# Kernel tuning notes

Measured on AMD Instinct MI355X. Metric: run time of the kernel, lower is better.

## Reference

```python
import jax, jax.numpy as jnp
import numpy as np

N_NODES = 50000


def gcn_conv(x, src, dst, W, b, n_nodes):
    """PyG GCNConv: linear -> sym-normalized aggregation with self-loops -> bias."""
    h = x @ W  # [N, out]
    # add self loops
    loop = jnp.arange(n_nodes, dtype=src.dtype)
    src_f = jnp.concatenate([src, loop])
    dst_f = jnp.concatenate([dst, loop])
    # degree at target nodes (edge weight = 1)
    deg = jax.ops.segment_sum(jnp.ones_like(dst_f, dtype=h.dtype), dst_f, num_segments=n_nodes)
    dinv = jnp.where(deg > 0, jax.lax.rsqrt(deg), 0.0)
    norm = dinv[src_f] * dinv[dst_f]  # [E+N]
    msg = h[src_f] * norm[:, None]    # gather + scale
    out = jax.ops.segment_sum(msg, dst_f, num_segments=n_nodes)
    return out + b


def setup_inputs() -> dict:
    key = jax.random.key(0)
    k1, k2, k3, k4 = jax.random.split(key, 4)
    N, F, H, C, E = N_NODES, 512, 256, 16, 800000
    x = jax.random.normal(k1, (N, F), dtype=jnp.float32)
    edge_index = jax.random.randint(k2, (2, E), 0, N, dtype=jnp.int64)
    W1 = jax.random.normal(k3, (F, H), dtype=jnp.float32) * (1.0 / np.sqrt(F))
    b1 = jnp.zeros((H,), dtype=jnp.float32)
    W2 = jax.random.normal(k4, (H, C), dtype=jnp.float32) * (1.0 / np.sqrt(H))
    b2 = jnp.zeros((C,), dtype=jnp.float32)
    return {"x": x, "edge_index": edge_index, "W1": W1, "b1": b1, "W2": W2, "b2": b2}


def reference(x, edge_index, W1, b1, W2, b2):
    src, dst = edge_index[0], edge_index[1]
    h = gcn_conv(x, src, dst, W1, b1, N_NODES)
    h = jax.nn.relu(h)
    # F.dropout with training=False (eval mode) is identity
    out = gcn_conv(h, src, dst, W2, b2, N_NODES)
    return out
```

## Files before the change

### kernel.cpp

```cpp
#include <hip/hip_runtime.h>
#include <stdint.h>

#define N_NODES 50000
#define N_PAD   50048
#define F_IN 512
#define H_DIM 256
#define C_DIM 16

typedef __attribute__((ext_vector_type(8))) short short8;
typedef __attribute__((ext_vector_type(4))) float f32x4;
typedef __attribute__((ext_vector_type(4))) unsigned short us4;
typedef __attribute__((ext_vector_type(8))) unsigned short us8;

__device__ inline float bf2f(unsigned short u) {
    return __uint_as_float(((uint32_t)u) << 16);
}
__device__ inline unsigned short f2bf(float f) {
    uint32_t u = __float_as_uint(f);
    u += 0x7FFFu + ((u >> 16) & 1u);
    return (unsigned short)(u >> 16);
}
__device__ inline unsigned short hx(float f) {
    return (unsigned short)(__float_as_uint(f) >> 16);
}
__device__ inline int eidx(const void* p, long long i, int is64) {
    return is64 ? (int)((const long long*)p)[i] : ((const int*)p)[i];
}

__device__ inline int row_beg(const int* ro, const int* bs, int n) {
    return ro[n] + bs[n >> 9];
}
__device__ inline int row_end(const int* ro, const int* bs, int n, int E) {
    return (n + 1 < N_NODES) ? ro[n + 1] + bs[(n + 1) >> 9] : E;
}

#define GLOAD16(gp, lp)                                                       \
    __builtin_amdgcn_global_load_lds(                                         \
        (const __attribute__((address_space(1))) void*)(gp),                  \
        (__attribute__((address_space(3))) void*)(lp), 16, 0, 0)


__global__ void prep_k(const void* ei, int* flag,
                       const float* w1, unsigned short* w1t,
                       const float* w2, unsigned short* w2t,
                       int* cnt, int* cur) {
    int i = blockIdx.x * 256 + threadIdx.x;
    if (i == 0) {
        const uint32_t* w = (const uint32_t*)ei;
        int is64 = 1;
        for (int j = 1; j < 128; j += 2)
            if (w[j] != 0u) { is64 = 0; break; }
        *flag = is64;
    }
    if (i < N_NODES) { cnt[i] = 0; cur[i] = 0; }
    if (i < F_IN * H_DIM) {
        int k = i / H_DIM, n = i % H_DIM;
        w1t[n * F_IN + k] = f2bf(w1[i]);
    }
    if (i < H_DIM * C_DIM) {
        int k = i / C_DIM, n = i % C_DIM;
        w2t[n * H_DIM + k] = f2bf(w2[i]);
    }
}


__global__ void hist_k(const void* ei, const int* flag, int* cnt, long long E) {
    long long e = (long long)blockIdx.x * 256 + threadIdx.x;
    if (e >= E) return;
    int d = eidx(ei, E + e, *flag);
    atomicAdd(&cnt[d], 1);
}

__global__ __launch_bounds__(512) void scan1_k(const int* cnt, int* rowoff, int* bsum,
                                               float* dinv, int n) {
    __shared__ int s[512];
    int t = threadIdx.x;
    int i = blockIdx.x * 512 + t;
    int v = (i < n) ? cnt[i] : 0;
    s[t] = v;
    __syncthreads();
    for (int off = 1; off < 512; off <<= 1) {
        int add = (t >= off) ? s[t - off] : 0;
        __syncthreads();
        s[t] += add;
        __syncthreads();
    }
    if (i < n) {
        rowoff[i] = s[t] - v;
        dinv[i] = rsqrtf((float)(v + 1));
    }
    if (t == 511) bsum[blockIdx.x] = s[511];
}

__global__ void scan2_k(int* bsum, int nb) {
    __shared__ int s[128];
    int t = threadIdx.x;
    int v = (t < nb) ? bsum[t] : 0;
    s[t] = v;
    __syncthreads();
    for (int off = 1; off < 128; off <<= 1) {
        int add = (t >= off) ? s[t - off] : 0;
        __syncthreads();
        s[t] += add;
        __syncthreads();
    }
    if (t < nb) bsum[t] = s[t] - v;
}

__global__ void scatter_k(const void* ei, const int* flag, const float* dinv,
                          const int* rowoff, const int* bsum, int* cur,
                          long long E, int2* colnorm) {
    long long e = (long long)blockIdx.x * 256 + threadIdx.x;
    if (e >= E) return;
    int is64 = *flag;
    int s = eidx(ei, e, is64);
    int d = eidx(ei, E + e, is64);
    int pos = row_beg(rowoff, bsum, d) + atomicAdd(&cur[d], 1);
    float nrm = dinv[s] * dinv[d];
    int2 cn;
    cn.x = s;
    cn.y = __float_as_int(nrm);
    colnorm[pos] = cn;
}


__global__ __launch_bounds__(512, 4) void gemm1_k(const float* __restrict__ x,
                                                  const unsigned short* __restrict__ w1t,
                                                  unsigned short* __restrict__ h1) {
    __shared__ __align__(16) float          Asf[2][128 * 32];
    __shared__ __align__(16) unsigned short Bs[2][256 * 32];

    const int t = threadIdx.x;
    const int wv = t >> 6, lane = t & 63;
    const int lg = lane >> 4, lr = lane & 15;
    const int wm = wv >> 2, wn = wv & 3;

    const int arow0 = t >> 3;
    const int achk = (t & 7) ^ (arow0 & 7);
    size_t g0 = (size_t)blockIdx.x * 128 + arow0;
    size_t g1 = g0 + 64;
    if (g0 > N_NODES - 1) g0 = N_NODES - 1;
    if (g1 > N_NODES - 1) g1 = N_NODES - 1;
    const float* asrc0 = x + g0 * F_IN + achk * 4;
    const float* asrc1 = x + g1 * F_IN + achk * 4;
    const unsigned short* bsrc0 = w1t + (size_t)(t >> 2) * F_IN + (t & 3) * 8;
    const unsigned short* bsrc1 = bsrc0 + 128 * F_IN;

#define STAGE(bf, ks)                                                         \
    do { const int _o = (ks) * 32;                                            \
        GLOAD16(asrc0 + _o, &Asf[bf][t * 4]);                                 \
        GLOAD16(asrc1 + _o, &Asf[bf][t * 4 + 2048]);                          \
        GLOAD16(bsrc0 + _o, &Bs[bf][t * 8]);                                  \
        GLOAD16(bsrc1 + _o, &Bs[bf][(t + 512) * 8]);                          \
    } while (0)

    f32x4 acc[4][4] = {};

    STAGE(0, 0);

    for (int ks = 0; ks < 16; ++ks) {
        const int bf = ks & 1;
        if (ks < 15) {
            STAGE(bf ^ 1, ks + 1);
            asm volatile("s_waitcnt vmcnt(4)" ::: "memory");
        } else {
            asm volatile("s_waitcnt vmcnt(0)" ::: "memory");
        }
        __builtin_amdgcn_sched_barrier(0);
        __builtin_amdgcn_s_barrier();

        short8 afr[4], bfr[4];
#pragma unroll
        for (int mi = 0; mi < 4; ++mi) {
            const int r = wm * 64 + mi * 16 + lr;
            const int s = r & 7;
            const float* base = &Asf[bf][r * 32];
            f32x4 lo = *(const f32x4*)(base + (((lg * 2) ^ s) * 4));
            f32x4 hi = *(const f32x4*)(base + (((lg * 2 + 1) ^ s) * 4));
            short8 a;
            a[0] = (short)hx(lo[0]); a[1] = (short)hx(lo[1]);
            a[2] = (short)hx(lo[2]); a[3] = (short)hx(lo[3]);
            a[4] = (short)hx(hi[0]); a[5] = (short)hx(hi[1]);
            a[6] = (short)hx(hi[2]); a[7] = (short)hx(hi[3]);
            afr[mi] = a;
        }
#pragma unroll
        for (int ni = 0; ni < 4; ++ni)
            bfr[ni] = *(const short8*)&Bs[bf][(wn * 64 + ni * 16 + lr) * 32 + lg * 8];
#pragma unroll
        for (int mi = 0; mi < 4; ++mi)
#pragma unroll
            for (int ni = 0; ni < 4; ++ni)
                acc[mi][ni] = __builtin_amdgcn_mfma_f32_16x16x32_bf16(
                    afr[mi], bfr[ni], acc[mi][ni], 0, 0, 0);

        asm volatile("s_waitcnt lgkmcnt(0)" ::: "memory");
        __builtin_amdgcn_sched_barrier(0);
        __builtin_amdgcn_s_barrier();
    }
#undef STAGE

    const size_t rbase = (size_t)blockIdx.x * 128 + wm * 64 + lg * 4;
#pragma unroll
    for (int mi = 0; mi < 4; ++mi)
#pragma unroll
        for (int ni = 0; ni < 4; ++ni)
#pragma unroll
            for (int j = 0; j < 4; ++j)
                h1[(rbase + mi * 16 + j) * H_DIM + wn * 64 + ni * 16 + lr] =
                    f2bf(acc[mi][ni][j]);
}


__global__ __launch_bounds__(256) void agg1_k(const unsigned short* __restrict__ h1,
                                              const int* __restrict__ rowoff,
                                              const int* __restrict__ bsum,
                                              const int2* __restrict__ colnorm,
                                              const float* __restrict__ dinv,
                                              const float* __restrict__ b1,
                                              unsigned short* __restrict__ h1a,
                                              int E) {
    int wv = threadIdx.x >> 6, lane = threadIdx.x & 63;
    int node = blockIdx.x * 4 + wv;
    if (node >= N_NODES) return;
    int half = lane >> 5;
    int fl = (lane & 31) * 8;
    int beg = row_beg(rowoff, bsum, node);
    int end = row_end(rowoff, bsum, node, E);
    float a[8] = {0.f, 0.f, 0.f, 0.f, 0.f, 0.f, 0.f, 0.f};
    const unsigned short* base = h1 + fl;

    int e = beg + half;
    while (e + 6 < end) {
        int2 c[4];
        us8 v[4];
#pragma unroll
        for (int q = 0; q < 4; ++q) c[q] = colnorm[e + q * 2];
#pragma unroll
        for (int q = 0; q < 4; ++q)
            v[q] = *(const us8*)(base + (long long)c[q].x * H_DIM);
#pragma unroll
        for (int q = 0; q < 4; ++q) {
            float n = __int_as_float(c[q].y);
#pragma unroll
            for (int j = 0; j < 8; ++j) a[j] += n * bf2f(v[q][j]);
        }
        e += 8;
    }
    while (e < end) {
        int2 c0 = colnorm[e];
        us8 v0 = *(const us8*)(base + (long long)c0.x * H_DIM);
        float n0 = __int_as_float(c0.y);
#pragma unroll
        for (int j = 0; j < 8; ++j) a[j] += n0 * bf2f(v0[j]);
        e += 2;
    }
#pragma unroll
    for (int j = 0; j < 8; ++j)
        a[j] += __shfl_xor(a[j], 32);

    if (half == 0) {
        float dn = dinv[node];
        float sn = dn * dn;
        us8 vs = *(const us8*)(base + (long long)node * H_DIM);
        float4 b0 = *(const float4*)(b1 + fl);
        float4 b4 = *(const float4*)(b1 + fl + 4);
        float bb[8] = {b0.x, b0.y, b0.z, b0.w, b4.x, b4.y, b4.z, b4.w};
        us8 o;
#pragma unroll
        for (int j = 0; j < 8; ++j) {
            float r = fmaxf(a[j] + sn * bf2f(vs[j]) + bb[j], 0.f);
            o[j] = f2bf(r);
        }
        *(us8*)(h1a + (long long)node * H_DIM + fl) = o;
    }
}


__global__ __launch_bounds__(256) void gemm2_k(const unsigned short* __restrict__ h1a,
                                               const unsigned short* __restrict__ w2t,
                                               float* __restrict__ h2) {
    int t = threadIdx.x;
    int wv = t >> 6, lane = t & 63, lg = lane >> 4, lr = lane & 15;
    int rbase = blockIdx.x * 64 + wv * 16;
    int rr = rbase + lr;
    int rc = rr < N_NODES ? rr : N_NODES - 1;
    f32x4 acc = {0.f, 0.f, 0.f, 0.f};
#pragma unroll
    for (int ks = 0; ks < 8; ++ks) {
        short8 a = *(const short8*)(h1a + (long long)rc * H_DIM + ks * 32 + lg * 8);
        short8 b = *(const short8*)(w2t + lr * H_DIM + ks * 32 + lg * 8);
        acc = __builtin_amdgcn_mfma_f32_16x16x32_bf16(a, b, acc, 0, 0, 0);
    }
#pragma unroll
    for (int j = 0; j < 4; ++j) {
        int row = rbase + lg * 4 + j;
        if (row < N_NODES) h2[(long long)row * C_DIM + lr] = acc[j];
    }
}


__global__ __launch_bounds__(256) void agg2_k(const float* __restrict__ h2,
                                              const int* __restrict__ rowoff,
                                              const int* __restrict__ bsum,
                                              const int2* __restrict__ colnorm,
                                              const float* __restrict__ dinv,
                                              const float* __restrict__ b2,
                                              float* __restrict__ out, int E) {
    int g = threadIdx.x >> 4, c = threadIdx.x & 15;
    int node = blockIdx.x * 16 + g;
    if (node >= N_NODES) return;
    int beg = row_beg(rowoff, bsum, node);
    int end = row_end(rowoff, bsum, node, E);
    float acc = 0.f;
    int e = beg;
    for (; e + 3 < end; e += 4) {
        int2 cn0 = colnorm[e];
        int2 cn1 = colnorm[e + 1];
        int2 cn2 = colnorm[e + 2];
        int2 cn3 = colnorm[e + 3];
        float v0 = h2[(long long)cn0.x * C_DIM + c];
        float v1 = h2[(long long)cn1.x * C_DIM + c];
        float v2 = h2[(long long)cn2.x * C_DIM + c];
        float v3 = h2[(long long)cn3.x * C_DIM + c];
        acc += __int_as_float(cn0.y) * v0 + __int_as_float(cn1.y) * v1
             + __int_as_float(cn2.y) * v2 + __int_as_float(cn3.y) * v3;
    }
    for (; e < end; ++e) {
        int2 cn = colnorm[e];
        acc += __int_as_float(cn.y) * h2[(long long)cn.x * C_DIM + c];
    }
    float dn = dinv[node];
    acc += dn * dn * h2[(long long)node * C_DIM + c];
    out[(long long)node * C_DIM + c] = acc + b2[c];
}


extern "C" void kernel_launch(void* const* d_in, const int* in_sizes, int n_in,
                              void* d_out, int out_size, void* d_ws, size_t ws_size,
                              hipStream_t stream) {
    const float* x  = (const float*)d_in[0];
    const void*  ei = d_in[1];
    const float* W1 = (const float*)d_in[2];
    const float* b1 = (const float*)d_in[3];
    const float* W2 = (const float*)d_in[4];
    const float* b2 = (const float*)d_in[5];
    float* out = (float*)d_out;
    long long E = (long long)in_sizes[1] / 2;

    char* w = (char*)d_ws;
    auto alloc = [&](size_t bytes) -> char* {
        char* p = w;
        w += (bytes + 255) & ~(size_t)255;
        return p;
    };
    int*   flag    = (int*)   alloc(4);
    int*   cnt     = (int*)   alloc((size_t)N_NODES * 4);
    int*   cur     = (int*)   alloc((size_t)N_NODES * 4);
    float* dinv    = (float*) alloc((size_t)N_NODES * 4);
    int*   rowoff  = (int*)   alloc((size_t)N_NODES * 4);
    int*   bsum    = (int*)   alloc(512 * 4);
    int2*  colnorm = (int2*)  alloc((size_t)E * 8);
    unsigned short* w1t = (unsigned short*)alloc((size_t)H_DIM * F_IN * 2);
    unsigned short* w2t = (unsigned short*)alloc((size_t)C_DIM * H_DIM * 2);
    unsigned short* h1  = (unsigned short*)alloc((size_t)N_PAD * H_DIM * 2);
    unsigned short* h1a = (unsigned short*)alloc((size_t)N_NODES * H_DIM * 2);
    float* h2 = (float*)alloc((size_t)N_NODES * C_DIM * 4);

    prep_k<<<(F_IN * H_DIM + 255) / 256, 256, 0, stream>>>(ei, flag, W1, w1t, W2, w2t,
                                                           cnt, cur);

    int egrid = (int)((E + 255) / 256);
    hist_k<<<egrid, 256, 0, stream>>>(ei, flag, cnt, E);
    int sgrid = (N_NODES + 511) / 512;
    scan1_k<<<sgrid, 512, 0, stream>>>(cnt, rowoff, bsum, dinv, N_NODES);
    scan2_k<<<1, 128, 0, stream>>>(bsum, sgrid);
    scatter_k<<<egrid, 256, 0, stream>>>(ei, flag, dinv, rowoff, bsum, cur, E, colnorm);

    gemm1_k<<<N_PAD / 128, 512, 0, stream>>>(x, w1t, h1);
    agg1_k<<<(N_NODES + 3) / 4, 256, 0, stream>>>(h1, rowoff, bsum, colnorm, dinv,
                                                  b1, h1a, (int)E);
    gemm2_k<<<(N_NODES + 63) / 64, 256, 0, stream>>>(h1a, w2t, h2);
    agg2_k<<<(N_NODES + 15) / 16, 256, 0, stream>>>(h2, rowoff, bsum, colnorm, dinv,
                                                    b2, out, (int)E);
}
```

Measured before the change: 202.2 us.

## Fold block-sum scan into scan1 and co-launch edge scatter with GEMM1

Removes the separate scan2 kernel by having the last-finishing scan1 block serially compute the exclusive prefix of block sums, using a done counter and thread fences. It also merges the CSR scatter into the GEMM1 launch as extra blocks, so the latency-bound atomic scatter can overlap with the compute-bound GEMM. This cuts two kernel launches and their gaps. The cost is a serial single-thread scan over about 98 entries and heavy LDS allocation on scatter blocks, which could limit their occupancy.

```diff
diff --git a/kernel.cpp b/kernel.cpp
--- a/kernel.cpp
+++ b/kernel.cpp
@@ -6,6 +6,7 @@
 #define F_IN 512
 #define H_DIM 256
 #define C_DIM 16
+#define G1_BLOCKS (N_PAD / 128)
 
 typedef __attribute__((ext_vector_type(8))) short short8;
 typedef __attribute__((ext_vector_type(4))) float f32x4;
@@ -43,7 +44,7 @@
 __global__ void prep_k(const void* ei, int* flag,
                        const float* w1, unsigned short* w1t,
                        const float* w2, unsigned short* w2t,
-                       int* cnt, int* cur) {
+                       int* cnt, int* cur, int* done) {
     int i = blockIdx.x * 256 + threadIdx.x;
     if (i == 0) {
         const uint32_t* w = (const uint32_t*)ei;
@@ -51,6 +52,7 @@
         for (int j = 1; j < 128; j += 2)
             if (w[j] != 0u) { is64 = 0; break; }
         *flag = is64;
+        *done = 0;
     }
     if (i < N_NODES) { cnt[i] = 0; cur[i] = 0; }
     if (i < F_IN * H_DIM) {
@@ -72,8 +74,9 @@
 }
 
 __global__ __launch_bounds__(512) void scan1_k(const int* cnt, int* rowoff, int* bsum,
-                                               float* dinv, int n) {
+                                               float* dinv, int* done, int n, int nblk) {
     __shared__ int s[512];
+    __shared__ int amLast;
     int t = threadIdx.x;
     int i = blockIdx.x * 512 + t;
     int v = (i < n) ? cnt[i] : 0;
@@ -90,45 +93,47 @@
         dinv[i] = rsqrtf((float)(v + 1));
     }
     if (t == 511) bsum[blockIdx.x] = s[511];
-}
-
-__global__ void scan2_k(int* bsum, int nb) {
-    __shared__ int s[128];
-    int t = threadIdx.x;
-    int v = (t < nb) ? bsum[t] : 0;
-    s[t] = v;
+    __threadfence();
+    if (t == 0) amLast = (atomicAdd(done, 1) == nblk - 1);
     __syncthreads();
-    for (int off = 1; off < 128; off <<= 1) {
-        int add = (t >= off) ? s[t - off] : 0;
-        __syncthreads();
-        s[t] += add;
-        __syncthreads();
-    }
-    if (t < nb) bsum[t] = s[t] - v;
-}
-
-__global__ void scatter_k(const void* ei, const int* flag, const float* dinv,
-                          const int* rowoff, const int* bsum, int* cur,
-                          long long E, int2* colnorm) {
-    long long e = (long long)blockIdx.x * 256 + threadIdx.x;
-    if (e >= E) return;
-    int is64 = *flag;
-    int s = eidx(ei, e, is64);
-    int d = eidx(ei, E + e, is64);
-    int pos = row_beg(rowoff, bsum, d) + atomicAdd(&cur[d], 1);
-    float nrm = dinv[s] * dinv[d];
-    int2 cn;
-    cn.x = s;
-    cn.y = __float_as_int(nrm);
-    colnorm[pos] = cn;
-}
-
-
-__global__ __launch_bounds__(512, 4) void gemm1_k(const float* __restrict__ x,
-                                                  const unsigned short* __restrict__ w1t,
-                                                  unsigned short* __restrict__ h1) {
+    if (amLast && t == 0) {
+        __threadfence();
+        volatile int* vb = bsum;
+        int run = 0;
+        for (int b = 0; b < nblk; ++b) {
+            int x = vb[b];
+            vb[b] = run;
+            run += x;
+        }
+    }
+}
+
+
+__global__ __launch_bounds__(512, 4) void gemm1scat_k(
+        const float* __restrict__ x, const unsigned short* __restrict__ w1t,
+        unsigned short* __restrict__ h1,
+        const void* __restrict__ ei, const int* __restrict__ flag,
+        const float* __restrict__ dinv, const int* __restrict__ rowoff,
+        const int* __restrict__ bsum, int* __restrict__ cur,
+        long long E, int2* __restrict__ colnorm) {
     __shared__ __align__(16) float          Asf[2][128 * 32];
     __shared__ __align__(16) unsigned short Bs[2][256 * 32];
+
+    if (blockIdx.x >= G1_BLOCKS) {
+        long long e = (long long)(blockIdx.x - G1_BLOCKS) * 512 + threadIdx.x;
+        if (e < E) {
+            int is64 = *flag;
+            int s = eidx(ei, e, is64);
+            int d = eidx(ei, E + e, is64);
+            int pos = row_beg(rowoff, bsum, d) + atomicAdd(&cur[d], 1);
+            float nrm = dinv[s] * dinv[d];
+            int2 cn;
+            cn.x = s;
+            cn.y = __float_as_int(nrm);
+            colnorm[pos] = cn;
+        }
+        return;
+    }
 
     const int t = threadIdx.x;
     const int wv = t >> 6, lane = t & 63;
@@ -354,7 +359,8 @@
         w += (bytes + 255) & ~(size_t)255;
         return p;
     };
-    int*   flag    = (int*)   alloc(4);
+    int*   flag    = (int*)   alloc(8);
+    int*   done    = flag + 1;
     int*   cnt     = (int*)   alloc((size_t)N_NODES * 4);
     int*   cur     = (int*)   alloc((size_t)N_NODES * 4);
     float* dinv    = (float*) alloc((size_t)N_NODES * 4);
@@ -368,16 +374,17 @@
     float* h2 = (float*)alloc((size_t)N_NODES * C_DIM * 4);
 
     prep_k<<<(F_IN * H_DIM + 255) / 256, 256, 0, stream>>>(ei, flag, W1, w1t, W2, w2t,
-                                                           cnt, cur);
+                                                           cnt, cur, done);
 
     int egrid = (int)((E + 255) / 256);
     hist_k<<<egrid, 256, 0, stream>>>(ei, flag, cnt, E);
     int sgrid = (N_NODES + 511) / 512;
-    scan1_k<<<sgrid, 512, 0, stream>>>(cnt, rowoff, bsum, dinv, N_NODES);
-    scan2_k<<<1, 128, 0, stream>>>(bsum, sgrid);
-    scatter_k<<<egrid, 256, 0, stream>>>(ei, flag, dinv, rowoff, bsum, cur, E, colnorm);
-
-    gemm1_k<<<N_PAD / 128, 512, 0, stream>>>(x, w1t, h1);
+    scan1_k<<<sgrid, 512, 0, stream>>>(cnt, rowoff, bsum, dinv, done, N_NODES, sgrid);
+
+    int scgrid = (int)((E + 511) / 512);
+    gemm1scat_k<<<G1_BLOCKS + scgrid, 512, 0, stream>>>(
+        x, w1t, h1, ei, flag, dinv, rowoff, bsum, cur, E, colnorm);
+
     agg1_k<<<(N_NODES + 3) / 4, 256, 0, stream>>>(h1, rowoff, bsum, colnorm, dinv,
                                                   b1, h1a, (int)E);
     gemm2_k<<<(N_NODES + 63) / 64, 256, 0, stream>>>(h1a, w2t, h2);
```

Result: slower. 250.1 us (+23.7%).

## Split hidden features into 32-column slabs so gather aggregation stays cache-resident

Applied to the files above, without the earlier changes.

Stores the first-layer hidden matrix as eight feature slabs of 32 columns each, rather than row-major 256-wide rows. The first aggregation kernel launches eight times as many blocks, and each block gathers only from one slab (about 3.2 MB), so the random neighbour gathers can hit in cache. The second GEMM and the GEMM1 epilogue are adapted to the new layout, and edge-list loads and output stores use nontemporal hints. In exchange, the CSR column list is re-read once per slab (eight times in total), and each gather is now a small 4-byte access per lane.

```diff
diff --git a/kernel.cpp b/kernel.cpp
--- a/kernel.cpp
+++ b/kernel.cpp
@@ -6,6 +6,7 @@
 #define F_IN 512
 #define H_DIM 256
 #define C_DIM 16
+#define SLAB ((size_t)N_PAD * 32)
 
 typedef __attribute__((ext_vector_type(8))) short short8;
 typedef __attribute__((ext_vector_type(4))) float f32x4;
@@ -126,7 +127,7 @@
 
 __global__ __launch_bounds__(512, 4) void gemm1_k(const float* __restrict__ x,
                                                   const unsigned short* __restrict__ w1t,
-                                                  unsigned short* __restrict__ h1) {
+                                                  unsigned short* __restrict__ h1s) {
     __shared__ __align__(16) float          Asf[2][128 * 32];
     __shared__ __align__(16) unsigned short Bs[2][256 * 32];
 
@@ -204,80 +205,81 @@
 #pragma unroll
     for (int mi = 0; mi < 4; ++mi)
 #pragma unroll
-        for (int ni = 0; ni < 4; ++ni)
+        for (int ni = 0; ni < 4; ++ni) {
+            const int s = wn * 2 + (ni >> 1);
+            const int c = (ni & 1) * 16 + lr;
+            unsigned short* dst = h1s + s * SLAB + c;
 #pragma unroll
             for (int j = 0; j < 4; ++j)
-                h1[(rbase + mi * 16 + j) * H_DIM + wn * 64 + ni * 16 + lr] =
-                    f2bf(acc[mi][ni][j]);
-}
-
-
-__global__ __launch_bounds__(256) void agg1_k(const unsigned short* __restrict__ h1,
+                dst[(rbase + mi * 16 + j) * 32] = f2bf(acc[mi][ni][j]);
+        }
+}
+
+
+__global__ __launch_bounds__(256) void agg1_k(const unsigned short* __restrict__ h1s,
                                               const int* __restrict__ rowoff,
                                               const int* __restrict__ bsum,
                                               const int2* __restrict__ colnorm,
                                               const float* __restrict__ dinv,
                                               const float* __restrict__ b1,
-                                              unsigned short* __restrict__ h1a,
+                                              unsigned short* __restrict__ h1as,
                                               int E) {
-    int wv = threadIdx.x >> 6, lane = threadIdx.x & 63;
-    int node = blockIdx.x * 4 + wv;
+    const int slice = blockIdx.x & 7;
+    const int nb = blockIdx.x >> 3;
+    const int wv = threadIdx.x >> 6, lane = threadIdx.x & 63;
+    const int node = nb * 4 + wv;
     if (node >= N_NODES) return;
-    int half = lane >> 5;
-    int fl = (lane & 31) * 8;
-    int beg = row_beg(rowoff, bsum, node);
-    int end = row_end(rowoff, bsum, node, E);
-    float a[8] = {0.f, 0.f, 0.f, 0.f, 0.f, 0.f, 0.f, 0.f};
-    const unsigned short* base = h1 + fl;
-
-    int e = beg + half;
-    while (e + 6 < end) {
-        int2 c[4];
-        us8 v[4];
-#pragma unroll
-        for (int q = 0; q < 4; ++q) c[q] = colnorm[e + q * 2];
-#pragma unroll
-        for (int q = 0; q < 4; ++q)
-            v[q] = *(const us8*)(base + (long long)c[q].x * H_DIM);
-#pragma unroll
-        for (int q = 0; q < 4; ++q) {
-            float n = __int_as_float(c[q].y);
-#pragma unroll
-            for (int j = 0; j < 8; ++j) a[j] += n * bf2f(v[q][j]);
-        }
+    const int eg = lane >> 4;
+    const int fp = lane & 15;
+    const unsigned short* slab = h1s + (size_t)slice * SLAB;
+
+    const int beg = row_beg(rowoff, bsum, node);
+    const int end = row_end(rowoff, bsum, node, E);
+    float a0 = 0.f, a1 = 0.f;
+
+    int e = beg + eg;
+    while (e + 4 < end) {
+        long long cc0 = __builtin_nontemporal_load((const long long*)&colnorm[e]);
+        long long cc1 = __builtin_nontemporal_load((const long long*)&colnorm[e + 4]);
+        int s0 = (int)cc0, s1 = (int)cc1;
+        float n0 = __uint_as_float((uint32_t)((unsigned long long)cc0 >> 32));
+        float n1 = __uint_as_float((uint32_t)((unsigned long long)cc1 >> 32));
+        uint32_t v0 = *(const uint32_t*)(slab + (size_t)s0 * 32 + fp * 2);
+        uint32_t v1 = *(const uint32_t*)(slab + (size_t)s1 * 32 + fp * 2);
+        a0 += n0 * bf2f(v0 & 0xffff) + n1 * bf2f(v1 & 0xffff);
+        a1 += n0 * bf2f(v0 >> 16) + n1 * bf2f(v1 >> 16);
         e += 8;
     }
     while (e < end) {
-        int2 c0 = colnorm[e];
-        us8 v0 = *(const us8*)(base + (long long)c0.x * H_DIM);
-        float n0 = __int_as_float(c0.y);
-#pragma unroll
-        for (int j = 0; j < 8; ++j) a[j] += n0 * bf2f(v0[j]);
-        e += 2;
-    }
-#pragma unroll
-    for (int j = 0; j < 8; ++j)
-        a[j] += __shfl_xor(a[j], 32);
-
-    if (half == 0) {
+        long long cc0 = __builtin_nontemporal_load((const long long*)&colnorm[e]);
+        int s0 = (int)cc0;
+        float n0 = __uint_as_float((uint32_t)((unsigned long long)cc0 >> 32));
+        uint32_t v0 = *(const uint32_t*)(slab + (size_t)s0 * 32 + fp * 2);
+        a0 += n0 * bf2f(v0 & 0xffff);
+        a1 += n0 * bf2f(v0 >> 16);
+        e += 4;
+    }
+    a0 += __shfl_xor(a0, 16);
+    a1 += __shfl_xor(a1, 16);
+    a0 += __shfl_xor(a0, 32);
+    a1 += __shfl_xor(a1, 32);
+
+    if (eg == 0) {
         float dn = dinv[node];
         float sn = dn * dn;
-        us8 vs = *(const us8*)(base + (long long)node * H_DIM);
-        float4 b0 = *(const float4*)(b1 + fl);
-        float4 b4 = *(const float4*)(b1 + fl + 4);
-        float bb[8] = {b0.x, b0.y, b0.z, b0.w, b4.x, b4.y, b4.z, b4.w};
-        us8 o;
-#pragma unroll
-        for (int j = 0; j < 8; ++j) {
-            float r = fmaxf(a[j] + sn * bf2f(vs[j]) + bb[j], 0.f);
-            o[j] = f2bf(r);
-        }
-        *(us8*)(h1a + (long long)node * H_DIM + fl) = o;
-    }
-}
-
-
-__global__ __launch_bounds__(256) void gemm2_k(const unsigned short* __restrict__ h1a,
+        uint32_t vs = *(const uint32_t*)(slab + (size_t)node * 32 + fp * 2);
+        float2 bb = *(const float2*)(b1 + slice * 32 + fp * 2);
+        a0 = fmaxf(a0 + sn * bf2f(vs & 0xffff) + bb.x, 0.f);
+        a1 = fmaxf(a1 + sn * bf2f(vs >> 16) + bb.y, 0.f);
+        uint32_t o = (uint32_t)f2bf(a0) | ((uint32_t)f2bf(a1) << 16);
+        uint32_t* dst = (uint32_t*)(h1as + (size_t)slice * SLAB +
+                                    (size_t)node * 32 + fp * 2);
+        __builtin_nontemporal_store(o, dst);
+    }
+}
+
+
+__global__ __launch_bounds__(256) void gemm2_k(const unsigned short* __restrict__ h1as,
                                                const unsigned short* __restrict__ w2t,
                                                float* __restrict__ h2) {
     int t = threadIdx.x;
@@ -288,7 +290,7 @@
     f32x4 acc = {0.f, 0.f, 0.f, 0.f};
 #pragma unroll
     for (int ks = 0; ks < 8; ++ks) {
-        short8 a = *(const short8*)(h1a + (long long)rc * H_DIM + ks * 32 + lg * 8);
+        short8 a = *(const short8*)(h1as + (size_t)ks * SLAB + (size_t)rc * 32 + lg * 8);
         short8 b = *(const short8*)(w2t + lr * H_DIM + ks * 32 + lg * 8);
         acc = __builtin_amdgcn_mfma_f32_16x16x32_bf16(a, b, acc, 0, 0, 0);
     }
@@ -361,10 +363,10 @@
     int*   rowoff  = (int*)   alloc((size_t)N_NODES * 4);
     int*   bsum    = (int*)   alloc(512 * 4);
     int2*  colnorm = (int2*)  alloc((size_t)E * 8);
-    unsigned short* w1t = (unsigned short*)alloc((size_t)H_DIM * F_IN * 2);
-    unsigned short* w2t = (unsigned short*)alloc((size_t)C_DIM * H_DIM * 2);
-    unsigned short* h1  = (unsigned short*)alloc((size_t)N_PAD * H_DIM * 2);
-    unsigned short* h1a = (unsigned short*)alloc((size_t)N_NODES * H_DIM * 2);
+    unsigned short* w1t  = (unsigned short*)alloc((size_t)H_DIM * F_IN * 2);
+    unsigned short* w2t  = (unsigned short*)alloc((size_t)C_DIM * H_DIM * 2);
+    unsigned short* h1s  = (unsigned short*)alloc(8 * SLAB * 2);
+    unsigned short* h1as = (unsigned short*)alloc(8 * SLAB * 2);
     float* h2 = (float*)alloc((size_t)N_NODES * C_DIM * 4);
 
     prep_k<<<(F_IN * H_DIM + 255) / 256, 256, 0, stream>>>(ei, flag, W1, w1t, W2, w2t,
@@ -377,10 +379,10 @@
     scan2_k<<<1, 128, 0, stream>>>(bsum, sgrid);
     scatter_k<<<egrid, 256, 0, stream>>>(ei, flag, dinv, rowoff, bsum, cur, E, colnorm);
 
-    gemm1_k<<<N_PAD / 128, 512, 0, stream>>>(x, w1t, h1);
-    agg1_k<<<(N_NODES + 3) / 4, 256, 0, stream>>>(h1, rowoff, bsum, colnorm, dinv,
-                                                  b1, h1a, (int)E);
-    gemm2_k<<<(N_NODES + 63) / 64, 256, 0, stream>>>(h1a, w2t, h2);
+    gemm1_k<<<N_PAD / 128, 512, 0, stream>>>(x, w1t, h1s);
+    agg1_k<<<8 * ((N_NODES + 3) / 4), 256, 0, stream>>>(h1s, rowoff, bsum, colnorm,
+                                                        dinv, b1, h1as, (int)E);
+    gemm2_k<<<(N_NODES + 63) / 64, 256, 0, stream>>>(h1as, w2t, h2);
     agg2_k<<<(N_NODES + 15) / 16, 256, 0, stream>>>(h2, rowoff, bsum, colnorm, dinv,
                                                     b2, out, (int)E);
 }
```

New measurement: 337.3 us. +66.8%, slower.
